# Kernel optimization log

Hardware: AMD Instinct MI355X
Metric: run time of the kernel (lower is better)

## Reference

```python
import jax, jax.numpy as jnp
import numpy as np

_EPS_COS = 1e-8  # F.cosine_similarity default eps
_EPS_ADD = 1e-12


def setup_inputs() -> dict:
    key = jax.random.key(0)
    ks = jax.random.split(key, 7)
    B, N, M, INT_SHIFT = 256, 4096, 64, 3
    return {
        "beta": jax.random.uniform(ks[0], (B, 1), dtype=jnp.float32),
        "kappa": jax.random.normal(ks[1], (B, M), dtype=jnp.float32),
        "gamma": jax.random.uniform(ks[2], (B, 1), dtype=jnp.float32),
        "g": jax.random.uniform(ks[3], (B, 1), dtype=jnp.float32),
        "s": jax.random.uniform(ks[4], (B, INT_SHIFT), dtype=jnp.float32),
        "w_prev": jax.random.uniform(ks[5], (B, N), dtype=jnp.float32),
        "memory": jax.random.normal(ks[6], (B, N, M), dtype=jnp.float32),
        "int_shift": INT_SHIFT,
    }


def reference(beta, kappa, gamma, g, s, w_prev, memory, int_shift):
    # --- content addressing: cosine similarity + softmax over N ---
    a = memory + _EPS_ADD                      # [B, N, M]
    b = kappa[:, None, :] + _EPS_ADD           # [B, 1, M]
    dot = jnp.einsum("bnm,bqm->bn", a, b)
    na = jnp.sqrt(jnp.sum(a * a, axis=-1))     # [B, N]
    nb = jnp.sqrt(jnp.sum(b * b, axis=-1))     # [B, 1]
    sim = dot / (jnp.maximum(na, _EPS_COS) * jnp.maximum(nb, _EPS_COS))
    w_c = jax.nn.softmax(beta * sim, axis=1)   # [B, N]

    # --- interpolate with previous weighting ---
    w_g = g * w_c + (1.0 - g) * w_prev         # [B, N]

    # --- circular shift: result[b, i] = sum_j s[b, j] * w_g[b, (i + j - 1) mod N]
    # (equivalent to the per-batch padded conv1d in the original, batched via roll)
    w_hat = jnp.zeros_like(w_g)
    for j in range(int_shift):
        w_hat = w_hat + s[:, j:j + 1] * jnp.roll(w_g, 1 - j, axis=1)

    # --- sharpen ---
    w = w_hat ** gamma
    w = w / (jnp.sum(w, axis=1, keepdims=True) + _EPS_ADD)
    return w
```

## Files before the change

kernel.cpp:

```cpp
#include <hip/hip_runtime.h>
#include <math.h>

#define EPS_COS 1e-8f
#define EPS_ADD 1e-12f


constexpr int NTHREADS = 1024;
constexpr int NWAVES   = NTHREADS / 64;
constexpr int MAX_N    = 4096;

__global__ __launch_bounds__(NTHREADS, 1) void ntm_attention_kernel(
    const float* __restrict__ beta,
    const float* __restrict__ kappa,
    const float* __restrict__ gamma,
    const float* __restrict__ g,
    const float* __restrict__ s,
    const float* __restrict__ w_prev,
    const float* __restrict__ mem,
    float* __restrict__ out,
    int N, int S)
{
    const int b    = blockIdx.x;
    const int tid  = threadIdx.x;
    const int lane = tid & 63;
    const int wave = tid >> 6;
    const int l16  = lane & 15;
    const int rgrp = lane >> 4;

    __shared__ float t_sh[MAX_N];
    __shared__ float w_sh[MAX_N];
    __shared__ float red[NWAVES];

    float4 kv = *reinterpret_cast<const float4*>(kappa + (size_t)b * 64 + l16 * 4);
    kv.x += EPS_ADD; kv.y += EPS_ADD; kv.z += EPS_ADD; kv.w += EPS_ADD;

    float nb2 = kv.x * kv.x + kv.y * kv.y + kv.z * kv.z + kv.w * kv.w;
#pragma unroll
    for (int m = 1; m < 16; m <<= 1) nb2 += __shfl_xor(nb2, m);
    const float nb = fmaxf(sqrtf(nb2), EPS_COS);
    const float bv = beta[b];

    const size_t base = (size_t)b * N * 64;
    float tmax = -INFINITY;

    const int nIter = N / 64;
    for (int it = 0; it < nIter; it += 4) {
        const int row0 = it * 64 + wave * 4 + rgrp;
        const float4* p = reinterpret_cast<const float4*>(mem + base + (size_t)row0 * 64) + l16;
        float4 a0 = p[0];
        float4 a1 = p[1024];
        float4 a2 = p[2048];
        float4 a3 = p[3072];

#pragma unroll
        for (int k = 0; k < 4; ++k) {
            float4 a = (k == 0) ? a0 : (k == 1) ? a1 : (k == 2) ? a2 : a3;
            a.x += EPS_ADD; a.y += EPS_ADD; a.z += EPS_ADD; a.w += EPS_ADD;
            float d  = a.x * kv.x + a.y * kv.y + a.z * kv.z + a.w * kv.w;
            float n2 = a.x * a.x + a.y * a.y + a.z * a.z + a.w * a.w;
#pragma unroll
            for (int m = 1; m < 16; m <<= 1) {
                d  += __shfl_xor(d, m);
                n2 += __shfl_xor(n2, m);
            }
            const float na = fmaxf(sqrtf(n2), EPS_COS);
            const float t  = bv * (d / (na * nb));
            const int row  = row0 + k * 64;
            if (l16 == 0) t_sh[row] = t;
            tmax = fmaxf(tmax, t);
        }
    }

#pragma unroll
    for (int m = 1; m < 64; m <<= 1) tmax = fmaxf(tmax, __shfl_xor(tmax, m));
    if (lane == 0) red[wave] = tmax;
    __syncthreads();
    float gmax = red[0];
#pragma unroll
    for (int i = 1; i < NWAVES; ++i) gmax = fmaxf(gmax, red[i]);
    __syncthreads();

    float lsum = 0.0f;
    for (int i = tid; i < N; i += NTHREADS) {
        const float e = expf(t_sh[i] - gmax);
        t_sh[i] = e;
        lsum += e;
    }
#pragma unroll
    for (int m = 1; m < 64; m <<= 1) lsum += __shfl_xor(lsum, m);
    if (lane == 0) red[wave] = lsum;
    __syncthreads();
    float tot = 0.0f;
#pragma unroll
    for (int i = 0; i < NWAVES; ++i) tot += red[i];
    __syncthreads();

    const float gv = g[b];
    for (int i = tid; i < N; i += NTHREADS) {
        const float wc = t_sh[i] / tot;
        const float wp = w_prev[(size_t)b * N + i];
        w_sh[i] = gv * wc + (1.0f - gv) * wp;
    }
    __syncthreads();

    const float gam = gamma[b];
    float sv[8];
    const int Sc = (S < 8) ? S : 8;
    for (int j = 0; j < Sc; ++j) sv[j] = s[(size_t)b * S + j];

    float ssum = 0.0f;
    for (int i = tid; i < N; i += NTHREADS) {
        float wh = 0.0f;
        for (int j = 0; j < Sc; ++j) {
            int idx = i + j - 1;
            idx += N;
            if (idx >= N) idx -= N;
            if (idx >= N) idx -= N;
            wh += sv[j] * w_sh[idx];
        }
        const float sh = powf(wh, gam);
        t_sh[i] = sh;
        ssum += sh;
    }
#pragma unroll
    for (int m = 1; m < 64; m <<= 1) ssum += __shfl_xor(ssum, m);
    if (lane == 0) red[wave] = ssum;
    __syncthreads();
    float stot = 0.0f;
#pragma unroll
    for (int i = 0; i < NWAVES; ++i) stot += red[i];

    const float denom = stot + EPS_ADD;
    for (int i = tid; i < N; i += NTHREADS) {
        out[(size_t)b * N + i] = t_sh[i] / denom;
    }
}

extern "C" void kernel_launch(void* const* d_in, const int* in_sizes, int n_in,
                              void* d_out, int out_size, void* d_ws, size_t ws_size,
                              hipStream_t stream) {
    const float* beta   = (const float*)d_in[0];
    const float* kappa  = (const float*)d_in[1];
    const float* gamma  = (const float*)d_in[2];
    const float* g      = (const float*)d_in[3];
    const float* s      = (const float*)d_in[4];
    const float* w_prev = (const float*)d_in[5];
    const float* mem    = (const float*)d_in[6];
    float* out          = (float*)d_out;

    const int B = in_sizes[0];
    const int N = in_sizes[5] / B;
    const int S = in_sizes[4] / B;

    ntm_attention_kernel<<<B, NTHREADS, 0, stream>>>(
        beta, kappa, gamma, g, s, w_prev, mem, out, N, S);
}
```

Baseline: 54.20 us.

## Fuse softmax exp into similarity pass, prefetch memory rows, vectorize tail stages

Computes exp of the scaled cosine similarity directly in the memory streaming loop, without subtracting a max. This drops one max-reduction, a barrier and one shared-memory pass. The memory loads are software-pipelined with a register double buffer, w_prev is loaded up front, the shift uses a power-of-two mask, and the later stages work on float4 per thread with one shared buffer. It drops the EPS_ADD on memory and hardcodes N == 4*NTHREADS and a power-of-two N. Skipping the max subtraction risks overflow when beta*sim is large.

```diff
diff --git a/kernel.cpp b/kernel.cpp
--- a/kernel.cpp
+++ b/kernel.cpp
@@ -4,12 +4,14 @@
 #define EPS_COS 1e-8f
 #define EPS_ADD 1e-12f
 
+typedef float f4 __attribute__((ext_vector_type(4)));
+
 
 constexpr int NTHREADS = 1024;
 constexpr int NWAVES   = NTHREADS / 64;
 constexpr int MAX_N    = 4096;
 
-__global__ __launch_bounds__(NTHREADS, 1) void ntm_attention_kernel(
+__global__ __launch_bounds__(NTHREADS, 1) void ntm_fused_kernel(
     const float* __restrict__ beta,
     const float* __restrict__ kappa,
     const float* __restrict__ gamma,
@@ -25,67 +27,53 @@
     const int lane = tid & 63;
     const int wave = tid >> 6;
     const int l16  = lane & 15;
-    const int rgrp = lane >> 4;
+    const int rg   = lane >> 4;
 
-    __shared__ float t_sh[MAX_N];
-    __shared__ float w_sh[MAX_N];
+    __shared__ float sh[MAX_N];
     __shared__ float red[NWAVES];
 
-    float4 kv = *reinterpret_cast<const float4*>(kappa + (size_t)b * 64 + l16 * 4);
-    kv.x += EPS_ADD; kv.y += EPS_ADD; kv.z += EPS_ADD; kv.w += EPS_ADD;
+    const f4 wp_reg = reinterpret_cast<const f4*>(w_prev + (size_t)b * N)[tid];
 
+    f4 kv = reinterpret_cast<const f4*>(kappa + (size_t)b * 64)[l16];
+    kv += (f4)EPS_ADD;
     float nb2 = kv.x * kv.x + kv.y * kv.y + kv.z * kv.z + kv.w * kv.w;
 #pragma unroll
     for (int m = 1; m < 16; m <<= 1) nb2 += __shfl_xor(nb2, m);
-    const float nb = fmaxf(sqrtf(nb2), EPS_COS);
-    const float bv = beta[b];
+    const float bscale = beta[b] / fmaxf(sqrtf(nb2), EPS_COS);
 
-    const size_t base = (size_t)b * N * 64;
-    float tmax = -INFINITY;
+    const int nRound = N >> 6;
+    const int row0   = wave * 4 + rg;
+    const f4* p = reinterpret_cast<const f4*>(mem + (size_t)b * N * 64)
+                  + (size_t)row0 * 16 + l16;
 
-    const int nIter = N / 64;
-    for (int it = 0; it < nIter; it += 4) {
-        const int row0 = it * 64 + wave * 4 + rgrp;
-        const float4* p = reinterpret_cast<const float4*>(mem + base + (size_t)row0 * 64) + l16;
-        float4 a0 = p[0];
-        float4 a1 = p[1024];
-        float4 a2 = p[2048];
-        float4 a3 = p[3072];
+    f4 a0 = p[0], a1 = p[1024], a2 = p[2048], a3 = p[3072];
+    float lsum = 0.0f;
 
+    for (int it = 0; it < nRound; it += 4) {
+        const f4 c0 = a0, c1 = a1, c2 = a2, c3 = a3;
+        if (it + 4 < nRound) {
+            const f4* pn = p + (size_t)(it + 4) * 1024;
+            a0 = pn[0]; a1 = pn[1024]; a2 = pn[2048]; a3 = pn[3072];
+        }
 #pragma unroll
-        for (int k = 0; k < 4; ++k) {
-            float4 a = (k == 0) ? a0 : (k == 1) ? a1 : (k == 2) ? a2 : a3;
-            a.x += EPS_ADD; a.y += EPS_ADD; a.z += EPS_ADD; a.w += EPS_ADD;
-            float d  = a.x * kv.x + a.y * kv.y + a.z * kv.z + a.w * kv.w;
-            float n2 = a.x * a.x + a.y * a.y + a.z * a.z + a.w * a.w;
+        for (int u = 0; u < 4; ++u) {
+            const f4 v = (u == 0) ? c0 : (u == 1) ? c1 : (u == 2) ? c2 : c3;
+            float d  = v.x * kv.x + v.y * kv.y + v.z * kv.z + v.w * kv.w;
+            float n2 = v.x * v.x + v.y * v.y + v.z * v.z + v.w * v.w;
 #pragma unroll
             for (int m = 1; m < 16; m <<= 1) {
                 d  += __shfl_xor(d, m);
                 n2 += __shfl_xor(n2, m);
             }
-            const float na = fmaxf(sqrtf(n2), EPS_COS);
-            const float t  = bv * (d / (na * nb));
-            const int row  = row0 + k * 64;
-            if (l16 == 0) t_sh[row] = t;
-            tmax = fmaxf(tmax, t);
+            const float t = bscale * d * rsqrtf(fmaxf(n2, 1e-16f));
+            const float e = expf(t);
+            if (l16 == 0) {
+                sh[row0 + (it + u) * 64] = e;
+                lsum += e;
+            }
         }
     }
 
-#pragma unroll
-    for (int m = 1; m < 64; m <<= 1) tmax = fmaxf(tmax, __shfl_xor(tmax, m));
-    if (lane == 0) red[wave] = tmax;
-    __syncthreads();
-    float gmax = red[0];
-#pragma unroll
-    for (int i = 1; i < NWAVES; ++i) gmax = fmaxf(gmax, red[i]);
-    __syncthreads();
-
-    float lsum = 0.0f;
-    for (int i = tid; i < N; i += NTHREADS) {
-        const float e = expf(t_sh[i] - gmax);
-        t_sh[i] = e;
-        lsum += e;
-    }
 #pragma unroll
     for (int m = 1; m < 64; m <<= 1) lsum += __shfl_xor(lsum, m);
     if (lane == 0) red[wave] = lsum;
@@ -93,13 +81,13 @@
     float tot = 0.0f;
 #pragma unroll
     for (int i = 0; i < NWAVES; ++i) tot += red[i];
-    __syncthreads();
 
     const float gv = g[b];
-    for (int i = tid; i < N; i += NTHREADS) {
-        const float wc = t_sh[i] / tot;
-        const float wp = w_prev[(size_t)b * N + i];
-        w_sh[i] = gv * wc + (1.0f - gv) * wp;
+    const float ws = gv / tot;
+    f4* sh4 = reinterpret_cast<f4*>(sh);
+    {
+        const f4 ev = sh4[tid];
+        sh4[tid] = ws * ev + (1.0f - gv) * wp_reg;
     }
     __syncthreads();
 
@@ -108,20 +96,21 @@
     const int Sc = (S < 8) ? S : 8;
     for (int j = 0; j < Sc; ++j) sv[j] = s[(size_t)b * S + j];
 
+    const int i0 = tid * 4;
+    const int mask = N - 1;
+    float o[4];
     float ssum = 0.0f;
-    for (int i = tid; i < N; i += NTHREADS) {
+#pragma unroll
+    for (int k = 0; k < 4; ++k) {
         float wh = 0.0f;
         for (int j = 0; j < Sc; ++j) {
-            int idx = i + j - 1;
-            idx += N;
-            if (idx >= N) idx -= N;
-            if (idx >= N) idx -= N;
-            wh += sv[j] * w_sh[idx];
+            const int idx = (i0 + k + j - 1) & mask;
+            wh += sv[j] * sh[idx];
         }
-        const float sh = powf(wh, gam);
-        t_sh[i] = sh;
-        ssum += sh;
+        o[k] = powf(wh, gam);
+        ssum += o[k];
     }
+
 #pragma unroll
     for (int m = 1; m < 64; m <<= 1) ssum += __shfl_xor(ssum, m);
     if (lane == 0) red[wave] = ssum;
@@ -130,10 +119,11 @@
 #pragma unroll
     for (int i = 0; i < NWAVES; ++i) stot += red[i];
 
-    const float denom = stot + EPS_ADD;
-    for (int i = tid; i < N; i += NTHREADS) {
-        out[(size_t)b * N + i] = t_sh[i] / denom;
-    }
+    const float inv_den = 1.0f / (stot + EPS_ADD);
+    f4 ov;
+    ov.x = o[0] * inv_den; ov.y = o[1] * inv_den;
+    ov.z = o[2] * inv_den; ov.w = o[3] * inv_den;
+    reinterpret_cast<f4*>(out + (size_t)b * N)[tid] = ov;
 }
 
 extern "C" void kernel_launch(void* const* d_in, const int* in_sizes, int n_in,
@@ -152,6 +142,6 @@
     const int N = in_sizes[5] / B;
     const int S = in_sizes[4] / B;
 
-    ntm_attention_kernel<<<B, NTHREADS, 0, stream>>>(
+    ntm_fused_kernel<<<B, NTHREADS, 0, stream>>>(
         beta, kappa, gamma, g, s, w_prev, mem, out, N, S);
 }
```

Measured after the change: 54.23 us. Within noise of the previous version (+0.1%).
